# Optimization experiments

Measured on AMD Instinct MI355X. Metric: run time of the kernel, lower is better.

The kernel has to match this reference:

```python
import jax, jax.numpy as jnp
import numpy as np

SIZES = [(64, 32), (32, 16), (16, 8), (8, 16), (16, 32)]
BZ, T, D = 2048, 512, 64


def setup_inputs() -> dict:
    key = jax.random.key(0)
    ks = jax.random.split(key, 32)
    inp = {
        "X": jax.random.normal(ks[0], (BZ, T, D), jnp.float32),
        "missing_mask": (jax.random.uniform(ks[1], (BZ, T, D)) < 0.8).astype(jnp.float32),
        "imputation_latent": jax.random.normal(ks[2], (BZ, T, D), jnp.float32),
    }
    for i, (din, dh) in enumerate(SIZES):
        s = 1.0 / np.sqrt(dh)  # PyTorch RNNCell init range
        k = 3 + 4 * i
        inp[f"wih{i}"] = jax.random.uniform(ks[k], (3 * dh, din), jnp.float32, -s, s)
        inp[f"whh{i}"] = jax.random.uniform(ks[k + 1], (3 * dh, dh), jnp.float32, -s, s)
        inp[f"bih{i}"] = jax.random.uniform(ks[k + 2], (3 * dh,), jnp.float32, -s, s)
        inp[f"bhh{i}"] = jax.random.uniform(ks[k + 3], (3 * dh,), jnp.float32, -s, s)
    so = 1.0 / np.sqrt(32)
    inp["out_w"] = jax.random.uniform(ks[23], (D, 32), jnp.float32, -so, so)
    inp["out_b"] = jax.random.uniform(ks[24], (D,), jnp.float32, -so, so)
    return inp


def _gru_cell(x, h, wih, whh, bih, bhh):
    # PyTorch nn.GRUCell gate order: r, z, n
    gi = x @ wih.T + bih
    gh = h @ whh.T + bhh
    ir, iz, inn = jnp.split(gi, 3, axis=-1)
    hr, hz, hn = jnp.split(gh, 3, axis=-1)
    r = jax.nn.sigmoid(ir + hr)
    z = jax.nn.sigmoid(iz + hz)
    n = jnp.tanh(inn + r * hn)
    return (1.0 - z) * n + z * h


def _forward(X, missing_mask, imputation_latent, params, out_w, out_b):
    imputed = X * missing_mask + imputation_latent * (1.0 - missing_mask)
    xs = jnp.swapaxes(imputed, 0, 1)  # [T, B, D]
    bz = X.shape[0]
    h0 = tuple(jnp.zeros((bz, dh), X.dtype) for _, dh in SIZES)

    def step(hs, x):
        new = []
        inp_x = x
        for i, (wih, whh, bih, bhh) in enumerate(params):
            h = _gru_cell(inp_x, hs[i], wih, whh, bih, bhh)
            new.append(h)
            inp_x = h  # layer i+1 consumes the freshly-updated hidden state
        return tuple(new), new[-1]

    _, hcol = jax.lax.scan(step, h0, xs)  # [T, B, 32]
    hcol = jnp.swapaxes(hcol, 0, 1)  # [B, T, 32]
    return hcol @ out_w.T + out_b


def reference(X, missing_mask, imputation_latent,
              wih0, whh0, bih0, bhh0, wih1, whh1, bih1, bhh1,
              wih2, whh2, bih2, bhh2, wih3, whh3, bih3, bhh3,
              wih4, whh4, bih4, bhh4, out_w, out_b):
    params = [(wih0, whh0, bih0, bhh0), (wih1, whh1, bih1, bhh1),
              (wih2, whh2, bih2, bhh2), (wih3, whh3, bih3, bhh3),
              (wih4, whh4, bih4, bhh4)]
    return _forward(X, missing_mask, imputation_latent, params, out_w, out_b)
```

## Files before the change

### kernel.cpp

```cpp
#include <hip/hip_runtime.h>

typedef short s16x8 __attribute__((ext_vector_type(8)));
typedef short s16x4 __attribute__((ext_vector_type(4)));
typedef float f32x4 __attribute__((ext_vector_type(4)));
typedef unsigned int u32;
typedef unsigned short u16;

#define NT 512
#define DD 64
#define BB 8
#define NTH 512

#define CHUNK 1024

#define P2STRIDE (5*CHUNK)
#define PH0 0
#define PH1 CHUNK
#define PH2 (2*CHUNK)
#define PH3 (3*CHUNK)
#define PH4 (4*CHUNK)
#define FRTOT2 (2*P2STRIDE)
#define NSTEP2 517

#define PSTRIDE (7*CHUNK)
#define XIN0 0
#define H0C (2*CHUNK)
#define H1C (3*CHUNK)
#define H2C (4*CHUNK)
#define H3C (5*CHUNK)
#define H4C (6*CHUNK)
#define FRTOT (2*PSTRIDE)
#define NSTEP_FB 517

#define MFMA16(A,B,C) __builtin_amdgcn_mfma_f32_16x16x32_bf16(A,B,C,0,0,0)

__device__ __forceinline__ float sigf(float x){ return 1.0f/(1.0f+__expf(-x)); }
__device__ __forceinline__ float tanhf2(float x){ return 2.0f/(1.0f+__expf(-2.0f*x)) - 1.0f; }

__device__ __forceinline__ u16 f2bf(float f) {
  u32 u = __builtin_bit_cast(u32, f);
  return (u16)((u + 0x7fffu + ((u >> 16) & 1u)) >> 16);
}
__device__ __forceinline__ float bf2f(u16 h) {
  u32 u = ((u32)h) << 16;
  return __builtin_bit_cast(float, u);
}

__device__ __forceinline__ void soft_barrier() {
  asm volatile("s_waitcnt lgkmcnt(0)" ::: "memory");
  __builtin_amdgcn_s_barrier();
  asm volatile("" ::: "memory");
}

__device__ __forceinline__ u32 cvtpk_bf16(float a, float b) {
  u32 r;
  asm("v_cvt_pk_bf16_f32 %0, %1, %2" : "=v"(r) : "v"(a), "v"(b));
  return r;
}

__device__ __forceinline__ void load_wfrag(const float* __restrict__ W, int row0, int nrow, int din,
                                           int kbase, int lane, s16x8& hi, s16x8& lo)
{
  const int m = lane & 15, kb = lane >> 4;
#pragma unroll
  for (int e = 0; e < 8; ++e) {
    int k = kbase + kb*8 + e;
    float v = (m < nrow && k < din) ? W[(size_t)(row0 + m)*din + k] : 0.0f;
    u16 h = f2bf(v);
    hi[e] = (short)h;
    lo[e] = (short)f2bf(v - bf2f(h));
  }
}

__device__ __forceinline__ void read_b(const u16* base, int lane, s16x8& hi, s16x8& lo)
{
  const int off = ((lane >> 4) << 8) + ((lane & 15) << 3);
  hi = *(const s16x8*)(base + off);
  lo = *(const s16x8*)(base + off + 128);
}

__device__ __forceinline__ void combine_write2(
    f32x4 aR, f32x4 aZ, f32x4 aNi, f32x4 aNh,
    float (&hprev)[4], u16* hdst_base, int jbase, int nrow, int lane)
{
  const int bb = lane & 15, q = lane >> 4;
  float hv[4];
#pragma unroll
  for (int i = 0; i < 4; ++i) {
    float rr = sigf(aR[i]);
    float zz = sigf(aZ[i]);
    float nn = tanhf2(aNi[i] + rr*aNh[i]);
    hv[i] = (1.0f - zz)*nn + zz*hprev[i];
    hprev[i] = hv[i];
  }
  if (bb < 8 && q*4 < nrow) {
    const int j = jbase + q*4;
    u16* dst = hdst_base + ((j >> 3) << 8) + bb*8 + (j & 7);
    u32 p01 = cvtpk_bf16(hv[0], hv[1]);
    u32 p23 = cvtpk_bf16(hv[2], hv[3]);
    float h0 = __builtin_bit_cast(float, p01 << 16);
    float h1 = __builtin_bit_cast(float, p01 & 0xffff0000u);
    float h2 = __builtin_bit_cast(float, p23 << 16);
    float h3 = __builtin_bit_cast(float, p23 & 0xffff0000u);
    u32 q01 = cvtpk_bf16(hv[0]-h0, hv[1]-h1);
    u32 q23 = cvtpk_bf16(hv[2]-h2, hv[3]-h3);
    uint2 hp_; hp_.x = p01; hp_.y = p23;
    uint2 lp_; lp_.x = q01; lp_.y = q23;
    *(uint2*)dst = hp_;
    *(uint2*)(dst + 128) = lp_;
  }
}

__device__ __forceinline__ void combine_write(
    f32x4 aR, f32x4 aZ, f32x4 aNi, f32x4 aNh,
    float (&hprev)[4], u16* hdst_base, int jbase, int nrow, int lane)
{
  const int bb = lane & 15, q = lane >> 4;
  float hv[4];
#pragma unroll
  for (int i = 0; i < 4; ++i) {
    float rr = sigf(aR[i]);
    float zz = sigf(aZ[i]);
    float nn = tanhf2(aNi[i] + rr*aNh[i]);
    hv[i] = (1.0f - zz)*nn + zz*hprev[i];
    hprev[i] = hv[i];
  }
  if (bb < 8 && q*4 < nrow) {
    const int j = jbase + q*4;
    const int kb = j >> 3, e = j & 7;
    s16x4 hh, ll;
#pragma unroll
    for (int i = 0; i < 4; ++i) {
      u16 h = f2bf(hv[i]);
      hh[i] = (short)h;
      ll[i] = (short)f2bf(hv[i] - bf2f(h));
    }
    u16* dst = hdst_base + kb*256 + bb*8 + e;
    *(s16x4*)dst = hh;
    *(s16x4*)(dst + 128) = ll;
  }
}

__global__ __launch_bounds__(256)
void gi0_gemm(const float* __restrict__ X, const float* __restrict__ M, const float* __restrict__ L,
              const float* __restrict__ wih0, const float* __restrict__ bih0,
              const float* __restrict__ bhh0,
              float* __restrict__ gi)
{
  __shared__ u32 xs[128*65];
  const int tid = threadIdx.x;
  const int wv = tid >> 6, lane = tid & 63;
  const int q = lane >> 4;
  const int b = blockIdx.x >> 2;
  const int t0 = (blockIdx.x & 3) * 128;
  const size_t base = ((size_t)b*NT + t0)*DD;

  for (int i = tid; i < 128*64; i += 256) {
    float x = X[base+i], m = M[base+i], l = L[base+i];
    float v = x*m + l*(1.0f - m);
    u16 h = f2bf(v);
    u16 lo2 = f2bf(v - bf2f(h));
    const int t = i >> 6, d = i & 63;
    xs[t*65 + d] = (u32)h | ((u32)lo2 << 16);
  }

  s16x8 Ah[6][2], Al[6][2];
  f32x4 cb[6];
#pragma unroll
  for (int tile = 0; tile < 6; ++tile) {
#pragma unroll
    for (int c = 0; c < 2; ++c)
      load_wfrag(wih0, tile*16, 16, 64, c*32, lane, Ah[tile][c], Al[tile][c]);
#pragma unroll
    for (int i = 0; i < 4; ++i) {
      int row = tile*16 + q*4 + i;
      float bv = bih0[row];
      if (tile < 4) bv += bhh0[row];
      cb[tile][i] = bv;
    }
  }
  __syncthreads();

#pragma unroll
  for (int g2 = 0; g2 < 2; ++g2) {
    const int tloc = g2*64 + wv*16 + (lane & 15);
    s16x8 Bh[2], Bl[2];
#pragma unroll
    for (int c = 0; c < 2; ++c) {
      const u32* p = &xs[tloc*65 + c*32 + q*8];
#pragma unroll
      for (int e = 0; e < 8; ++e) {
        u32 v = p[e];
        Bh[c][e] = (short)(v & 0xffffu);
        Bl[c][e] = (short)(v >> 16);
      }
    }
    float* gp = gi + ((size_t)b*NT + t0 + tloc)*96 + q*4;
#pragma unroll
    for (int tile = 0; tile < 6; ++tile) {
      f32x4 acc = cb[tile];
#pragma unroll
      for (int c = 0; c < 2; ++c) {
        acc = MFMA16(Ah[tile][c], Bh[c], acc);
        acc = MFMA16(Ah[tile][c], Bl[c], acc);
        acc = MFMA16(Al[tile][c], Bh[c], acc);
      }
      *(f32x4*)(gp + tile*16) = acc;
    }
  }
}

__device__ __forceinline__ void wave_l0(
    const float* __restrict__ Whh, const float* __restrict__ bhh,
    const float* __restrict__ gi, int jbase,
    u16* FRu, int b0, int lane)
{
  s16x8 Ahh[3], Ahl[3];
#pragma unroll
  for (int g = 0; g < 3; ++g)
    load_wfrag(Whh, g*32 + jbase, 16, 32, 0, lane, Ahh[g], Ahl[g]);
  const int q = lane >> 4;
  f32x4 cNh;
#pragma unroll
  for (int i = 0; i < 4; ++i) cNh[i] = bhh[64 + jbase + q*4 + i];
  float hprev[4] = {0.f,0.f,0.f,0.f};

  const float* gp = gi + (size_t)(b0 + (lane & 7)) * ((size_t)NT*96) + jbase + q*4;
  f32x4 gR0, gZ0, gN0, gR1, gZ1, gN1;
  gR0 = *(const f32x4*)(gp); gZ0 = *(const f32x4*)(gp+32); gN0 = *(const f32x4*)(gp+64); gp += 96;
  gR1 = *(const f32x4*)(gp); gZ1 = *(const f32x4*)(gp+32); gN1 = *(const f32x4*)(gp+64); gp += 96;

  for (int s = 0; s < NSTEP2; ++s) {
    const int par = s & 1, rp = par ^ 1;
    f32x4 gR2 = {}, gZ2 = {}, gN2 = {};
    if (s + 2 < NT) {
      gR2 = *(const f32x4*)(gp); gZ2 = *(const f32x4*)(gp+32); gN2 = *(const f32x4*)(gp+64); gp += 96;
    }
    if (s < NT) {
      f32x4 aR = gR0, aZ = gZ0, aNi = gN0, aNh = cNh;
      s16x8 bh_, bl_;
      read_b(FRu + rp*P2STRIDE + PH0, lane, bh_, bl_);
      aR  = MFMA16(Ahh[0], bh_, aR);  aR  = MFMA16(Ahh[0], bl_, aR);  aR  = MFMA16(Ahl[0], bh_, aR);
      aZ  = MFMA16(Ahh[1], bh_, aZ);  aZ  = MFMA16(Ahh[1], bl_, aZ);  aZ  = MFMA16(Ahl[1], bh_, aZ);
      aNh = MFMA16(Ahh[2], bh_, aNh); aNh = MFMA16(Ahh[2], bl_, aNh); aNh = MFMA16(Ahl[2], bh_, aNh);
      combine_write2(aR, aZ, aNi, aNh, hprev, FRu + par*P2STRIDE + PH0, jbase, 16, lane);
    }
    gR0 = gR1; gZ0 = gZ1; gN0 = gN1;
    gR1 = gR2; gZ1 = gZ2; gN1 = gN2;
    soft_barrier();
  }
}

template<int DIN, int DH>
__device__ __forceinline__ void wave_mid(
    const float* __restrict__ Wih, const float* __restrict__ Whh,
    const float* __restrict__ bih, const float* __restrict__ bhh,
    int jbase, int xc, int hc, int s0, int s1,
    u16* FRu, int b0, int lane)
{
  const int nrow = (DH - jbase) < 16 ? (DH - jbase) : 16;
  s16x8 Axh[3], Axl[3], Ahh[3], Ahl[3];
#pragma unroll
  for (int g = 0; g < 3; ++g) {
    load_wfrag(Wih, g*DH + jbase, nrow, DIN, 0, lane, Axh[g], Axl[g]);
    load_wfrag(Whh, g*DH + jbase, nrow, DH, 0, lane, Ahh[g], Ahl[g]);
  }
  const int q = lane >> 4;
  f32x4 cR, cZ, cNi, cNh;
#pragma unroll
  for (int i = 0; i < 4; ++i) {
    int lr = q*4 + i;
    int j = jbase + lr;
    bool jr = lr < nrow;
    cR[i]  = jr ? bih[j] + bhh[j] : 0.f;
    cZ[i]  = jr ? bih[DH+j] + bhh[DH+j] : 0.f;
    cNi[i] = jr ? bih[2*DH+j] : 0.f;
    cNh[i] = jr ? bhh[2*DH+j] : 0.f;
  }
  float hprev[4] = {0.f,0.f,0.f,0.f};

  for (int s = 0; s < NSTEP2; ++s) {
    const int par = s & 1, rp = par ^ 1;
    if (s >= s0 && s <= s1) {
      f32x4 aR = cR, aZ = cZ, aNi = cNi, aNh = cNh;
      s16x8 bh_, bl_;
      read_b(FRu + rp*P2STRIDE + xc, lane, bh_, bl_);
      aR  = MFMA16(Axh[0], bh_, aR);  aR  = MFMA16(Axh[0], bl_, aR);  aR  = MFMA16(Axl[0], bh_, aR);
      aZ  = MFMA16(Axh[1], bh_, aZ);  aZ  = MFMA16(Axh[1], bl_, aZ);  aZ  = MFMA16(Axl[1], bh_, aZ);
      aNi = MFMA16(Axh[2], bh_, aNi); aNi = MFMA16(Axh[2], bl_, aNi); aNi = MFMA16(Axl[2], bh_, aNi);
      read_b(FRu + rp*P2STRIDE + hc, lane, bh_, bl_);
      aR  = MFMA16(Ahh[0], bh_, aR);  aR  = MFMA16(Ahh[0], bl_, aR);  aR  = MFMA16(Ahl[0], bh_, aR);
      aZ  = MFMA16(Ahh[1], bh_, aZ);  aZ  = MFMA16(Ahh[1], bl_, aZ);  aZ  = MFMA16(Ahl[1], bh_, aZ);
      aNh = MFMA16(Ahh[2], bh_, aNh); aNh = MFMA16(Ahh[2], bl_, aNh); aNh = MFMA16(Ahl[2], bh_, aNh);
      combine_write2(aR, aZ, aNi, aNh, hprev, FRu + par*P2STRIDE + hc, jbase, nrow, lane);
    }
    soft_barrier();
  }
}

__device__ __forceinline__ void wave_out2(
    const float* __restrict__ OW, const float* __restrict__ OBb,
    u16* FRu, float* __restrict__ out, int b0, int lane)
{
  s16x8 Oh[4], Ol[4];
  f32x4 cO[4];
  const int q = lane >> 4, bb = lane & 15;
#pragma unroll
  for (int t4 = 0; t4 < 4; ++t4) {
    load_wfrag(OW, t4*16, 16, 32, 0, lane, Oh[t4], Ol[t4]);
#pragma unroll
    for (int i = 0; i < 4; ++i) cO[t4][i] = OBb[t4*16 + q*4 + i];
  }
  float* op = out + ((size_t)(b0 + (bb & 7))*NT)*DD + q*4;

  for (int s = 0; s < NSTEP2; ++s) {
    const int rp = (s & 1) ^ 1;
    if (s >= 5) {
      s16x8 bh_, bl_;
      read_b(FRu + rp*P2STRIDE + PH4, lane, bh_, bl_);
#pragma unroll
      for (int t4 = 0; t4 < 4; ++t4) {
        f32x4 a_ = cO[t4];
        a_ = MFMA16(Oh[t4], bh_, a_); a_ = MFMA16(Oh[t4], bl_, a_); a_ = MFMA16(Ol[t4], bh_, a_);
        if (bb < 8) *(f32x4*)(op + t4*16) = a_;
      }
      op += DD;
    }
    soft_barrier();
  }
}

__global__ __launch_bounds__(NTH, 1)
void gru_rec(const float* __restrict__ gi,
             const float* __restrict__ whh0, const float* __restrict__ bhh0,
             const float* __restrict__ wih1, const float* __restrict__ whh1, const float* __restrict__ bih1, const float* __restrict__ bhh1,
             const float* __restrict__ wih2, const float* __restrict__ whh2, const float* __restrict__ bih2, const float* __restrict__ bhh2,
             const float* __restrict__ wih3, const float* __restrict__ whh3, const float* __restrict__ bih3, const float* __restrict__ bhh3,
             const float* __restrict__ wih4, const float* __restrict__ whh4, const float* __restrict__ bih4, const float* __restrict__ bhh4,
             const float* __restrict__ out_w, const float* __restrict__ out_b,
             float* __restrict__ out)
{
  __shared__ __align__(16) u16 FRu[FRTOT2];
  const int tid = threadIdx.x;
  const int w = tid >> 6, lane = tid & 63;
  const int b0 = blockIdx.x * BB;

  for (int i = tid; i < FRTOT2; i += NTH) FRu[i] = 0;
  __syncthreads();

  if (w == 0)
    wave_l0(whh0, bhh0, gi,  0, FRu, b0, lane);
  else if (w == 1)
    wave_l0(whh0, bhh0, gi, 16, FRu, b0, lane);
  else if (w == 2)
    wave_mid<32,16>(wih1,whh1,bih1,bhh1,  0, PH0, PH1, 1, 512, FRu, b0, lane);
  else if (w == 4)
    wave_mid<16, 8>(wih2,whh2,bih2,bhh2,  0, PH1, PH2, 2, 513, FRu, b0, lane);
  else if (w == 5)
    wave_mid< 8,16>(wih3,whh3,bih3,bhh3,  0, PH2, PH3, 3, 514, FRu, b0, lane);
  else if (w == 3)
    wave_mid<16,32>(wih4,whh4,bih4,bhh4,  0, PH3, PH4, 4, 515, FRu, b0, lane);
  else if (w == 6)
    wave_mid<16,32>(wih4,whh4,bih4,bhh4, 16, PH3, PH4, 4, 515, FRu, b0, lane);
  else
    wave_out2(out_w, out_b, FRu, out, b0, lane);
}

__device__ __forceinline__ void write_x(u16* FRu, int par, int w, int lane, float v)
{
  const int d = lane;
  const int chunk = d >> 5, kb = (d >> 3) & 3, e = d & 7;
  u16 h = f2bf(v);
  u16 l2 = f2bf(v - bf2f(h));
  u16* p = FRu + par*PSTRIDE + XIN0 + chunk*CHUNK + kb*256 + w*8 + e;
  p[0] = h; p[128] = l2;
}

template<int DIN, int DH, int NXC>
__device__ __forceinline__ void wave_gru_fb(
    const float* __restrict__ Wih, const float* __restrict__ Whh,
    const float* __restrict__ bih, const float* __restrict__ bhh,
    int jbase, int xc, int hc, int s0, int s1,
    u16* FRu, float* OST,
    const float* __restrict__ X, const float* __restrict__ Mm, const float* __restrict__ Ll,
    float* __restrict__ out, int b0, int w, int lane)
{
  const int nrow = (DH - jbase) < 16 ? (DH - jbase) : 16;
  s16x8 Axh[3][NXC], Axl[3][NXC], Ahh[3], Ahl[3];
#pragma unroll
  for (int g = 0; g < 3; ++g) {
#pragma unroll
    for (int c = 0; c < NXC; ++c)
      load_wfrag(Wih, g*DH + jbase, nrow, DIN, c*32, lane, Axh[g][c], Axl[g][c]);
    load_wfrag(Whh, g*DH + jbase, nrow, DH, 0, lane, Ahh[g], Ahl[g]);
  }
  f32x4 cR, cZ, cNi, cNh;
  {
    const int q = lane >> 4;
#pragma unroll
    for (int i = 0; i < 4; ++i) {
      int lr = q*4 + i;
      int j = jbase + lr;
      bool jr = lr < nrow;
      cR[i]  = jr ? bih[j] + bhh[j] : 0.f;
      cZ[i]  = jr ? bih[DH+j] + bhh[DH+j] : 0.f;
      cNi[i] = jr ? bih[2*DH+j] : 0.f;
      cNh[i] = jr ? bhh[2*DH+j] : 0.f;
    }
  }
  float hprev[4] = {0.f, 0.f, 0.f, 0.f};

  const size_t gbase = ((size_t)(b0 + w))*((size_t)NT*DD) + lane;
  float rx = X[gbase], rm = Mm[gbase], rl = Ll[gbase];
  write_x(FRu, 1, w, lane, rx*rm + rl*(1.0f - rm));
  rx = X[gbase + DD]; rm = Mm[gbase + DD]; rl = Ll[gbase + DD];
  __syncthreads();

  for (int s = 0; s < NSTEP_FB; ++s) {
    const int par = s & 1, rp = par ^ 1;
    float nx = 0.f, nm = 0.f, nl = 0.f;
    if (s <= 509) {
      size_t g = gbase + (size_t)(s+2)*DD;
      nx = X[g]; nm = Mm[g]; nl = Ll[g];
    }
    f32x4 aR = cR, aZ = cZ, aNi = cNi, aNh = cNh;
    const bool run = (s >= s0) && (s <= s1);
    if (run) {
      const u16* RB = FRu + rp*PSTRIDE;
      s16x8 bh_, bl_;
#pragma unroll
      for (int c = 0; c < NXC; ++c) {
        read_b(RB + xc + c*CHUNK, lane, bh_, bl_);
        aR  = MFMA16(Axh[0][c], bh_, aR);  aR  = MFMA16(Axh[0][c], bl_, aR);  aR  = MFMA16(Axl[0][c], bh_, aR);
        aZ  = MFMA16(Axh[1][c], bh_, aZ);  aZ  = MFMA16(Axh[1][c], bl_, aZ);  aZ  = MFMA16(Axl[1][c], bh_, aZ);
        aNi = MFMA16(Axh[2][c], bh_, aNi); aNi = MFMA16(Axh[2][c], bl_, aNi); aNi = MFMA16(Axl[2][c], bh_, aNi);
      }
      read_b(RB + hc, lane, bh_, bl_);
      aR  = MFMA16(Ahh[0], bh_, aR);  aR  = MFMA16(Ahh[0], bl_, aR);  aR  = MFMA16(Ahl[0], bh_, aR);
      aZ  = MFMA16(Ahh[1], bh_, aZ);  aZ  = MFMA16(Ahh[1], bl_, aZ);  aZ  = MFMA16(Ahl[1], bh_, aZ);
      aNh = MFMA16(Ahh[2], bh_, aNh); aNh = MFMA16(Ahh[2], bl_, aNh); aNh = MFMA16(Ahl[2], bh_, aNh);
    }
    __syncthreads();

    if (run)
      combine_write(aR, aZ, aNi, aNh, hprev, FRu + par*PSTRIDE + hc, jbase, nrow, lane);
    if (s >= 5)
      out[((size_t)(b0 + w)*NT + (s-5))*DD + lane] = OST[w*65 + lane];
    if (s <= 510) write_x(FRu, par, w, lane, rx*rm + rl*(1.0f - rm));
    rx = nx; rm = nm; rl = nl;
    __syncthreads();
  }
}

__device__ __forceinline__ void wave_out_fb(
    const float* __restrict__ OW, const float* __restrict__ OBb,
    u16* FRu, float* OST,
    const float* __restrict__ X, const float* __restrict__ Mm, const float* __restrict__ Ll,
    float* __restrict__ out, int b0, int w, int lane)
{
  s16x8 Oh[4], Ol[4];
  f32x4 cO[4];
#pragma unroll
  for (int t4 = 0; t4 < 4; ++t4) {
    load_wfrag(OW, t4*16, 16, 32, 0, lane, Oh[t4], Ol[t4]);
#pragma unroll
    for (int i = 0; i < 4; ++i) cO[t4][i] = OBb[t4*16 + (lane>>4)*4 + i];
  }
  const size_t gbase = ((size_t)(b0 + w))*((size_t)NT*DD) + lane;
  float rx = X[gbase], rm = Mm[gbase], rl = Ll[gbase];
  write_x(FRu, 1, w, lane, rx*rm + rl*(1.0f - rm));
  rx = X[gbase + DD]; rm = Mm[gbase + DD]; rl = Ll[gbase + DD];
  __syncthreads();

  for (int s = 0; s < NSTEP_FB; ++s) {
    const int par = s & 1, rp = par ^ 1;
    float nx = 0.f, nm = 0.f, nl = 0.f;
    if (s <= 509) { size_t g = gbase + (size_t)(s+2)*DD; nx = X[g]; nm = Mm[g]; nl = Ll[g]; }
    if (s >= 5) {
      s16x8 bh_, bl_;
      read_b(FRu + rp*PSTRIDE + H4C, lane, bh_, bl_);
      const int bb = lane & 15, q = lane >> 4;
#pragma unroll
      for (int t4 = 0; t4 < 4; ++t4) {
        f32x4 a_ = cO[t4];
        a_ = MFMA16(Oh[t4], bh_, a_); a_ = MFMA16(Oh[t4], bl_, a_); a_ = MFMA16(Ol[t4], bh_, a_);
        if (bb < 8) {
#pragma unroll
          for (int i = 0; i < 4; ++i) OST[bb*65 + t4*16 + q*4 + i] = a_[i];
        }
      }
    }
    __syncthreads();
    if (s >= 5)
      out[((size_t)(b0 + w)*NT + (s-5))*DD + lane] = OST[w*65 + lane];
    if (s <= 510) write_x(FRu, par, w, lane, rx*rm + rl*(1.0f - rm));
    rx = nx; rm = nm; rl = nl;
    __syncthreads();
  }
}

__global__ __launch_bounds__(NTH, 1)
void gru_mfma(const float* __restrict__ X, const float* __restrict__ M, const float* __restrict__ L,
              const float* __restrict__ wih0, const float* __restrict__ whh0, const float* __restrict__ bih0, const float* __restrict__ bhh0,
              const float* __restrict__ wih1, const float* __restrict__ whh1, const float* __restrict__ bih1, const float* __restrict__ bhh1,
              const float* __restrict__ wih2, const float* __restrict__ whh2, const float* __restrict__ bih2, const float* __restrict__ bhh2,
              const float* __restrict__ wih3, const float* __restrict__ whh3, const float* __restrict__ bih3, const float* __restrict__ bhh3,
              const float* __restrict__ wih4, const float* __restrict__ whh4, const float* __restrict__ bih4, const float* __restrict__ bhh4,
              const float* __restrict__ out_w, const float* __restrict__ out_b,
              float* __restrict__ out)
{
  __shared__ __align__(16) u16 FRu[FRTOT];
  __shared__ float OST[8*65];
  const int tid = threadIdx.x;
  const int w = tid >> 6, lane = tid & 63;
  const int b0 = blockIdx.x * BB;

  for (int i = tid; i < FRTOT; i += NTH) FRu[i] = 0;
  for (int i = tid; i < 8*65; i += NTH) OST[i] = 0.f;
  __syncthreads();

  if (w == 0)
    wave_gru_fb<64,32,2>(wih0,whh0,bih0,bhh0,  0, XIN0, H0C, 0, 511, FRu, OST, X,M,L, out, b0, w, lane);
  else if (w == 1)
    wave_gru_fb<64,32,2>(wih0,whh0,bih0,bhh0, 16, XIN0, H0C, 0, 511, FRu, OST, X,M,L, out, b0, w, lane);
  else if (w == 2)
    wave_gru_fb<32,16,1>(wih1,whh1,bih1,bhh1,  0, H0C,  H1C, 1, 512, FRu, OST, X,M,L, out, b0, w, lane);
  else if (w == 4)
    wave_gru_fb<16, 8,1>(wih2,whh2,bih2,bhh2,  0, H1C,  H2C, 2, 513, FRu, OST, X,M,L, out, b0, w, lane);
  else if (w == 5)
    wave_gru_fb< 8,16,1>(wih3,whh3,bih3,bhh3,  0, H2C,  H3C, 3, 514, FRu, OST, X,M,L, out, b0, w, lane);
  else if (w == 3)
    wave_gru_fb<16,32,1>(wih4,whh4,bih4,bhh4,  0, H3C,  H4C, 4, 515, FRu, OST, X,M,L, out, b0, w, lane);
  else if (w == 6)
    wave_gru_fb<16,32,1>(wih4,whh4,bih4,bhh4, 16, H3C,  H4C, 4, 515, FRu, OST, X,M,L, out, b0, w, lane);
  else
    wave_out_fb(out_w, out_b, FRu, OST, X,M,L, out, b0, w, lane);
}

extern "C" void kernel_launch(void* const* d_in, const int* in_sizes, int n_in,
                              void* d_out, int out_size, void* d_ws, size_t ws_size,
                              hipStream_t stream)
{
  const float* X  = (const float*)d_in[0];
  const float* M  = (const float*)d_in[1];
  const float* L  = (const float*)d_in[2];
  const float* wp[20];
  for (int i = 0; i < 20; ++i) wp[i] = (const float*)d_in[3 + i];
  const float* ow = (const float*)d_in[23];
  const float* ob = (const float*)d_in[24];
  float* out = (float*)d_out;

  const size_t gi_bytes = (size_t)2048 * NT * 96 * sizeof(float);
  if (ws_size >= gi_bytes) {
    float* gi = (float*)d_ws;
    gi0_gemm<<<dim3(2048*4), dim3(256), 0, stream>>>(X, M, L, wp[0], wp[2], wp[3], gi);
    gru_rec<<<dim3(2048 / BB), dim3(NTH), 0, stream>>>(
        gi, wp[1], wp[3],
        wp[4], wp[5], wp[6], wp[7],
        wp[8], wp[9], wp[10], wp[11],
        wp[12], wp[13], wp[14], wp[15],
        wp[16], wp[17], wp[18], wp[19],
        ow, ob, out);
  } else {
    gru_mfma<<<dim3(2048 / BB), dim3(NTH), 0, stream>>>(
        X, M, L,
        wp[0], wp[1], wp[2], wp[3],
        wp[4], wp[5], wp[6], wp[7],
        wp[8], wp[9], wp[10], wp[11],
        wp[12], wp[13], wp[14], wp[15],
        wp[16], wp[17], wp[18], wp[19],
        ow, ob, out);
  }
}
```

Baseline: 840.1 us.

## Split recurrence into 4-batch, 4-wave blocks with lane-swizzled gate combine

Each recurrent block now handles 4 batch rows with 4 waves instead of 8 rows with 8 waves, launching 512 blocks with two blocks per CU. Each wave now runs several layer tiles: layer 0 as two tiles, layers 1+2, layers 3 plus half of layer 4, and the other half of layer 4 plus the output projection. The combine step uses ds_swizzle so the upper half of the lanes processes accumulator rows 2-3, which avoids idle lanes when only 4 batch columns are live. The aim is to double the number of blocks and give more CUs work, at the cost of more serial MFMA work per wave on each timestep.

Result: slower. 1.016 ms (+21.0%).

```diff
diff --git a/kernel.cpp b/kernel.cpp
--- a/kernel.cpp
+++ b/kernel.cpp
@@ -8,7 +8,6 @@
 
 #define NT 512
 #define DD 64
-#define BB 8
 #define NTH 512
 
 #define CHUNK 1024
@@ -58,6 +57,11 @@
   return r;
 }
 
+__device__ __forceinline__ float swzf(float v) {
+  return __builtin_bit_cast(float,
+      __builtin_amdgcn_ds_swizzle(__builtin_bit_cast(int, v), 0x201F));
+}
+
 __device__ __forceinline__ void load_wfrag(const float* __restrict__ W, int row0, int nrow, int din,
                                            int kbase, int lane, s16x8& hi, s16x8& lo)
 {
@@ -79,66 +83,92 @@
   lo = *(const s16x8*)(base + off + 128);
 }
 
-__device__ __forceinline__ void combine_write2(
+template<bool NI_OWN>
+__device__ __forceinline__ void combine_split(
     f32x4 aR, f32x4 aZ, f32x4 aNi, f32x4 aNh,
-    float (&hprev)[4], u16* hdst_base, int jbase, int nrow, int lane)
+    float (&hp)[2], u16* dstC, int jt16, int nrow, int lane)
 {
   const int bb = lane & 15, q = lane >> 4;
-  float hv[4];
+  const bool hihalf = (bb & 8) != 0;
+  float sR2 = swzf(aR[2]), sR3 = swzf(aR[3]);
+  float sZ2 = swzf(aZ[2]), sZ3 = swzf(aZ[3]);
+  float sH2 = swzf(aNh[2]), sH3 = swzf(aNh[3]);
+  float r0 = hihalf ? sR2 : aR[0],  r1 = hihalf ? sR3 : aR[1];
+  float z0 = hihalf ? sZ2 : aZ[0],  z1 = hihalf ? sZ3 : aZ[1];
+  float nh0 = hihalf ? sH2 : aNh[0], nh1 = hihalf ? sH3 : aNh[1];
+  float ni0, ni1;
+  if (NI_OWN) {
+    ni0 = hihalf ? aNi[2] : aNi[0];
+    ni1 = hihalf ? aNi[3] : aNi[1];
+  } else {
+    float sN2 = swzf(aNi[2]), sN3 = swzf(aNi[3]);
+    ni0 = hihalf ? sN2 : aNi[0];
+    ni1 = hihalf ? sN3 : aNi[1];
+  }
+  float rr0 = sigf(r0), rr1 = sigf(r1);
+  float zz0 = sigf(z0), zz1 = sigf(z1);
+  float n0 = tanhf2(ni0 + rr0*nh0), n1 = tanhf2(ni1 + rr1*nh1);
+  float h0 = (1.0f - zz0)*n0 + zz0*hp[0];
+  float h1 = (1.0f - zz1)*n1 + zz1*hp[1];
+  hp[0] = h0; hp[1] = h1;
+  const int jj = q*4 + (hihalf ? 2 : 0);
+  if ((bb & 7) < 4 && jj < nrow) {
+    const int j = jt16 + jj;
+    u32 ph = cvtpk_bf16(h0, h1);
+    float f0 = h0 - __builtin_bit_cast(float, ph << 16);
+    float f1 = h1 - __builtin_bit_cast(float, ph & 0xffff0000u);
+    u32 pl = cvtpk_bf16(f0, f1);
+    u16* dst = dstC + ((j >> 3) << 8) + ((bb & 3) << 3) + (j & 7);
+    *(u32*)dst = ph;
+    *(u32*)(dst + 128) = pl;
+  }
+}
+
+struct WTile {
+  s16x8 Axh[3], Axl[3], Ahh[3], Ahl[3];
+  f32x4 cR, cZ, cNi, cNh;
+};
+
+__device__ __forceinline__ void load_tile(WTile& w,
+    const float* __restrict__ Wih, const float* __restrict__ Whh,
+    const float* __restrict__ bih, const float* __restrict__ bhh,
+    int jbase, int DH, int DIN, int nrow, int lane)
+{
+#pragma unroll
+  for (int g = 0; g < 3; ++g) {
+    load_wfrag(Wih, g*DH + jbase, nrow, DIN, 0, lane, w.Axh[g], w.Axl[g]);
+    load_wfrag(Whh, g*DH + jbase, nrow, DH, 0, lane, w.Ahh[g], w.Ahl[g]);
+  }
+  const int q = lane >> 4;
 #pragma unroll
   for (int i = 0; i < 4; ++i) {
-    float rr = sigf(aR[i]);
-    float zz = sigf(aZ[i]);
-    float nn = tanhf2(aNi[i] + rr*aNh[i]);
-    hv[i] = (1.0f - zz)*nn + zz*hprev[i];
-    hprev[i] = hv[i];
-  }
-  if (bb < 8 && q*4 < nrow) {
-    const int j = jbase + q*4;
-    u16* dst = hdst_base + ((j >> 3) << 8) + bb*8 + (j & 7);
-    u32 p01 = cvtpk_bf16(hv[0], hv[1]);
-    u32 p23 = cvtpk_bf16(hv[2], hv[3]);
-    float h0 = __builtin_bit_cast(float, p01 << 16);
-    float h1 = __builtin_bit_cast(float, p01 & 0xffff0000u);
-    float h2 = __builtin_bit_cast(float, p23 << 16);
-    float h3 = __builtin_bit_cast(float, p23 & 0xffff0000u);
-    u32 q01 = cvtpk_bf16(hv[0]-h0, hv[1]-h1);
-    u32 q23 = cvtpk_bf16(hv[2]-h2, hv[3]-h3);
-    uint2 hp_; hp_.x = p01; hp_.y = p23;
-    uint2 lp_; lp_.x = q01; lp_.y = q23;
-    *(uint2*)dst = hp_;
-    *(uint2*)(dst + 128) = lp_;
-  }
-}
-
-__device__ __forceinline__ void combine_write(
-    f32x4 aR, f32x4 aZ, f32x4 aNi, f32x4 aNh,
-    float (&hprev)[4], u16* hdst_base, int jbase, int nrow, int lane)
-{
-  const int bb = lane & 15, q = lane >> 4;
-  float hv[4];
-#pragma unroll
-  for (int i = 0; i < 4; ++i) {
-    float rr = sigf(aR[i]);
-    float zz = sigf(aZ[i]);
-    float nn = tanhf2(aNi[i] + rr*aNh[i]);
-    hv[i] = (1.0f - zz)*nn + zz*hprev[i];
-    hprev[i] = hv[i];
-  }
-  if (bb < 8 && q*4 < nrow) {
-    const int j = jbase + q*4;
-    const int kb = j >> 3, e = j & 7;
-    s16x4 hh, ll;
-#pragma unroll
-    for (int i = 0; i < 4; ++i) {
-      u16 h = f2bf(hv[i]);
-      hh[i] = (short)h;
-      ll[i] = (short)f2bf(hv[i] - bf2f(h));
-    }
-    u16* dst = hdst_base + kb*256 + bb*8 + e;
-    *(s16x4*)dst = hh;
-    *(s16x4*)(dst + 128) = ll;
-  }
+    int lr = q*4 + i, j = jbase + lr;
+    bool jr = lr < nrow;
+    w.cR[i]  = jr ? bih[j] + bhh[j] : 0.f;
+    w.cZ[i]  = jr ? bih[DH+j] + bhh[DH+j] : 0.f;
+    w.cNi[i] = jr ? bih[2*DH+j] : 0.f;
+    w.cNh[i] = jr ? bhh[2*DH+j] : 0.f;
+  }
+}
+
+__device__ __forceinline__ void do_mid_tile(const WTile& w,
+    const u16* bx, const u16* bhc, u16* dstC,
+    float (&hp)[2], int jt16, int nrow, int lane)
+{
+  s16x8 bh_, bl_;
+  read_b(bx, lane, bh_, bl_);
+  f32x4 aR  = MFMA16(w.Axh[0], bh_, w.cR);
+  aR  = MFMA16(w.Axh[0], bl_, aR);  aR  = MFMA16(w.Axl[0], bh_, aR);
+  f32x4 aZ  = MFMA16(w.Axh[1], bh_, w.cZ);
+  aZ  = MFMA16(w.Axh[1], bl_, aZ);  aZ  = MFMA16(w.Axl[1], bh_, aZ);
+  f32x4 aNi = MFMA16(w.Axh[2], bh_, w.cNi);
+  aNi = MFMA16(w.Axh[2], bl_, aNi); aNi = MFMA16(w.Axl[2], bh_, aNi);
+  read_b(bhc, lane, bh_, bl_);
+  aR  = MFMA16(w.Ahh[0], bh_, aR);  aR  = MFMA16(w.Ahh[0], bl_, aR);  aR  = MFMA16(w.Ahl[0], bh_, aR);
+  aZ  = MFMA16(w.Ahh[1], bh_, aZ);  aZ  = MFMA16(w.Ahh[1], bl_, aZ);  aZ  = MFMA16(w.Ahl[1], bh_, aZ);
+  f32x4 aNh = MFMA16(w.Ahh[2], bh_, w.cNh);
+  aNh = MFMA16(w.Ahh[2], bl_, aNh); aNh = MFMA16(w.Ahl[2], bh_, aNh);
+  combine_split<false>(aR, aZ, aNi, aNh, hp, dstC, jt16, nrow, lane);
 }
 
 __global__ __launch_bounds__(256)
@@ -210,98 +240,130 @@
   }
 }
 
-__device__ __forceinline__ void wave_l0(
-    const float* __restrict__ Whh, const float* __restrict__ bhh,
-    const float* __restrict__ gi, int jbase,
-    u16* FRu, int b0, int lane)
-{
-  s16x8 Ahh[3], Ahl[3];
-#pragma unroll
-  for (int g = 0; g < 3; ++g)
-    load_wfrag(Whh, g*32 + jbase, 16, 32, 0, lane, Ahh[g], Ahl[g]);
+__device__ void wv_l0(const float* __restrict__ whh0, const float* __restrict__ bhh0,
+                      const float* __restrict__ gi, u16* FR, int b0, int lane)
+{
+  s16x8 Ahh[2][3], Ahl[2][3];
+#pragma unroll
+  for (int jt = 0; jt < 2; ++jt)
+#pragma unroll
+    for (int g = 0; g < 3; ++g)
+      load_wfrag(whh0, g*32 + jt*16, 16, 32, 0, lane, Ahh[jt][g], Ahl[jt][g]);
   const int q = lane >> 4;
-  f32x4 cNh;
-#pragma unroll
-  for (int i = 0; i < 4; ++i) cNh[i] = bhh[64 + jbase + q*4 + i];
-  float hprev[4] = {0.f,0.f,0.f,0.f};
-
-  const float* gp = gi + (size_t)(b0 + (lane & 7)) * ((size_t)NT*96) + jbase + q*4;
-  f32x4 gR0, gZ0, gN0, gR1, gZ1, gN1;
-  gR0 = *(const f32x4*)(gp); gZ0 = *(const f32x4*)(gp+32); gN0 = *(const f32x4*)(gp+64); gp += 96;
-  gR1 = *(const f32x4*)(gp); gZ1 = *(const f32x4*)(gp+32); gN1 = *(const f32x4*)(gp+64); gp += 96;
+  f32x4 cNh[2];
+#pragma unroll
+  for (int jt = 0; jt < 2; ++jt)
+#pragma unroll
+    for (int i = 0; i < 4; ++i) cNh[jt][i] = bhh0[64 + jt*16 + q*4 + i];
+  float hp[2][2] = {{0.f,0.f},{0.f,0.f}};
+
+  const float* gp = gi + (size_t)(b0 + (lane & 3)) * ((size_t)NT*96) + q*4;
+  f32x4 g0[2][3], g1[2][3];
+#pragma unroll
+  for (int jt = 0; jt < 2; ++jt) {
+    g0[jt][0] = *(const f32x4*)(gp + jt*16);
+    g0[jt][1] = *(const f32x4*)(gp + 32 + jt*16);
+    g0[jt][2] = *(const f32x4*)(gp + 64 + jt*16);
+  }
+  gp += 96;
+#pragma unroll
+  for (int jt = 0; jt < 2; ++jt) {
+    g1[jt][0] = *(const f32x4*)(gp + jt*16);
+    g1[jt][1] = *(const f32x4*)(gp + 32 + jt*16);
+    g1[jt][2] = *(const f32x4*)(gp + 64 + jt*16);
+  }
+  gp += 96;
 
   for (int s = 0; s < NSTEP2; ++s) {
     const int par = s & 1, rp = par ^ 1;
-    f32x4 gR2 = {}, gZ2 = {}, gN2 = {};
+    f32x4 g2[2][3];
+#pragma unroll
+    for (int jt = 0; jt < 2; ++jt)
+#pragma unroll
+      for (int g = 0; g < 3; ++g) g2[jt][g] = f32x4{0.f,0.f,0.f,0.f};
     if (s + 2 < NT) {
-      gR2 = *(const f32x4*)(gp); gZ2 = *(const f32x4*)(gp+32); gN2 = *(const f32x4*)(gp+64); gp += 96;
+#pragma unroll
+      for (int jt = 0; jt < 2; ++jt) {
+        g2[jt][0] = *(const f32x4*)(gp + jt*16);
+        g2[jt][1] = *(const f32x4*)(gp + 32 + jt*16);
+        g2[jt][2] = *(const f32x4*)(gp + 64 + jt*16);
+      }
+      gp += 96;
     }
     if (s < NT) {
-      f32x4 aR = gR0, aZ = gZ0, aNi = gN0, aNh = cNh;
       s16x8 bh_, bl_;
-      read_b(FRu + rp*P2STRIDE + PH0, lane, bh_, bl_);
-      aR  = MFMA16(Ahh[0], bh_, aR);  aR  = MFMA16(Ahh[0], bl_, aR);  aR  = MFMA16(Ahl[0], bh_, aR);
-      aZ  = MFMA16(Ahh[1], bh_, aZ);  aZ  = MFMA16(Ahh[1], bl_, aZ);  aZ  = MFMA16(Ahl[1], bh_, aZ);
-      aNh = MFMA16(Ahh[2], bh_, aNh); aNh = MFMA16(Ahh[2], bl_, aNh); aNh = MFMA16(Ahl[2], bh_, aNh);
-      combine_write2(aR, aZ, aNi, aNh, hprev, FRu + par*P2STRIDE + PH0, jbase, 16, lane);
-    }
-    gR0 = gR1; gZ0 = gZ1; gN0 = gN1;
-    gR1 = gR2; gZ1 = gZ2; gN1 = gN2;
+      read_b(FR + rp*P2STRIDE + PH0, lane, bh_, bl_);
+#pragma unroll
+      for (int jt = 0; jt < 2; ++jt) {
+        f32x4 aR  = MFMA16(Ahh[jt][0], bh_, g0[jt][0]);
+        aR  = MFMA16(Ahh[jt][0], bl_, aR);  aR  = MFMA16(Ahl[jt][0], bh_, aR);
+        f32x4 aZ  = MFMA16(Ahh[jt][1], bh_, g0[jt][1]);
+        aZ  = MFMA16(Ahh[jt][1], bl_, aZ);  aZ  = MFMA16(Ahl[jt][1], bh_, aZ);
+        f32x4 aNh = MFMA16(Ahh[jt][2], bh_, cNh[jt]);
+        aNh = MFMA16(Ahh[jt][2], bl_, aNh); aNh = MFMA16(Ahl[jt][2], bh_, aNh);
+        combine_split<true>(aR, aZ, g0[jt][2], aNh, hp[jt],
+                            FR + par*P2STRIDE + PH0, jt*16, 16, lane);
+      }
+    }
+#pragma unroll
+    for (int jt = 0; jt < 2; ++jt)
+#pragma unroll
+      for (int g = 0; g < 3; ++g) { g0[jt][g] = g1[jt][g]; g1[jt][g] = g2[jt][g]; }
     soft_barrier();
   }
 }
 
-template<int DIN, int DH>
-__device__ __forceinline__ void wave_mid(
-    const float* __restrict__ Wih, const float* __restrict__ Whh,
-    const float* __restrict__ bih, const float* __restrict__ bhh,
-    int jbase, int xc, int hc, int s0, int s1,
-    u16* FRu, int b0, int lane)
-{
-  const int nrow = (DH - jbase) < 16 ? (DH - jbase) : 16;
-  s16x8 Axh[3], Axl[3], Ahh[3], Ahl[3];
-#pragma unroll
-  for (int g = 0; g < 3; ++g) {
-    load_wfrag(Wih, g*DH + jbase, nrow, DIN, 0, lane, Axh[g], Axl[g]);
-    load_wfrag(Whh, g*DH + jbase, nrow, DH, 0, lane, Ahh[g], Ahl[g]);
-  }
-  const int q = lane >> 4;
-  f32x4 cR, cZ, cNi, cNh;
-#pragma unroll
-  for (int i = 0; i < 4; ++i) {
-    int lr = q*4 + i;
-    int j = jbase + lr;
-    bool jr = lr < nrow;
-    cR[i]  = jr ? bih[j] + bhh[j] : 0.f;
-    cZ[i]  = jr ? bih[DH+j] + bhh[DH+j] : 0.f;
-    cNi[i] = jr ? bih[2*DH+j] : 0.f;
-    cNh[i] = jr ? bhh[2*DH+j] : 0.f;
-  }
-  float hprev[4] = {0.f,0.f,0.f,0.f};
-
+__device__ void wv_l1_l2(
+    const float* __restrict__ wih1, const float* __restrict__ whh1,
+    const float* __restrict__ bih1, const float* __restrict__ bhh1,
+    const float* __restrict__ wih2, const float* __restrict__ whh2,
+    const float* __restrict__ bih2, const float* __restrict__ bhh2,
+    u16* FR, int lane)
+{
+  WTile t1, t2;
+  load_tile(t1, wih1, whh1, bih1, bhh1, 0, 16, 32, 16, lane);
+  load_tile(t2, wih2, whh2, bih2, bhh2, 0,  8, 16,  8, lane);
+  float hp1[2] = {0.f,0.f}, hp2[2] = {0.f,0.f};
   for (int s = 0; s < NSTEP2; ++s) {
     const int par = s & 1, rp = par ^ 1;
-    if (s >= s0 && s <= s1) {
-      f32x4 aR = cR, aZ = cZ, aNi = cNi, aNh = cNh;
-      s16x8 bh_, bl_;
-      read_b(FRu + rp*P2STRIDE + xc, lane, bh_, bl_);
-      aR  = MFMA16(Axh[0], bh_, aR);  aR  = MFMA16(Axh[0], bl_, aR);  aR  = MFMA16(Axl[0], bh_, aR);
-      aZ  = MFMA16(Axh[1], bh_, aZ);  aZ  = MFMA16(Axh[1], bl_, aZ);  aZ  = MFMA16(Axl[1], bh_, aZ);
-      aNi = MFMA16(Axh[2], bh_, aNi); aNi = MFMA16(Axh[2], bl_, aNi); aNi = MFMA16(Axl[2], bh_, aNi);
-      read_b(FRu + rp*P2STRIDE + hc, lane, bh_, bl_);
-      aR  = MFMA16(Ahh[0], bh_, aR);  aR  = MFMA16(Ahh[0], bl_, aR);  aR  = MFMA16(Ahl[0], bh_, aR);
-      aZ  = MFMA16(Ahh[1], bh_, aZ);  aZ  = MFMA16(Ahh[1], bl_, aZ);  aZ  = MFMA16(Ahl[1], bh_, aZ);
-      aNh = MFMA16(Ahh[2], bh_, aNh); aNh = MFMA16(Ahh[2], bl_, aNh); aNh = MFMA16(Ahl[2], bh_, aNh);
-      combine_write2(aR, aZ, aNi, aNh, hprev, FRu + par*P2STRIDE + hc, jbase, nrow, lane);
-    }
+    const u16* R = FR + rp*P2STRIDE;
+    u16* W = FR + par*P2STRIDE;
+    if (s >= 1 && s <= 512) do_mid_tile(t1, R+PH0, R+PH1, W+PH1, hp1, 0, 16, lane);
+    if (s >= 2 && s <= 513) do_mid_tile(t2, R+PH1, R+PH2, W+PH2, hp2, 0,  8, lane);
     soft_barrier();
   }
 }
 
-__device__ __forceinline__ void wave_out2(
+__device__ void wv_l3_l4b(
+    const float* __restrict__ wih3, const float* __restrict__ whh3,
+    const float* __restrict__ bih3, const float* __restrict__ bhh3,
+    const float* __restrict__ wih4, const float* __restrict__ whh4,
+    const float* __restrict__ bih4, const float* __restrict__ bhh4,
+    u16* FR, int lane)
+{
+  WTile t3, t4b;
+  load_tile(t3,  wih3, whh3, bih3, bhh3,  0, 16,  8, 16, lane);
+  load_tile(t4b, wih4, whh4, bih4, bhh4, 16, 32, 16, 16, lane);
+  float hp3[2] = {0.f,0.f}, hp4[2] = {0.f,0.f};
+  for (int s = 0; s < NSTEP2; ++s) {
+    const int par = s & 1, rp = par ^ 1;
+    const u16* R = FR + rp*P2STRIDE;
+    u16* W = FR + par*P2STRIDE;
+    if (s >= 3 && s <= 514) do_mid_tile(t3,  R+PH2, R+PH3, W+PH3, hp3,  0, 16, lane);
+    if (s >= 4 && s <= 515) do_mid_tile(t4b, R+PH3, R+PH4, W+PH4, hp4, 16, 16, lane);
+    soft_barrier();
+  }
+}
+
+__device__ void wv_l4a_out(
+    const float* __restrict__ wih4, const float* __restrict__ whh4,
+    const float* __restrict__ bih4, const float* __restrict__ bhh4,
     const float* __restrict__ OW, const float* __restrict__ OBb,
-    u16* FRu, float* __restrict__ out, int b0, int lane)
-{
+    u16* FR, float* __restrict__ out, int b0, int lane)
+{
+  WTile t4a;
+  load_tile(t4a, wih4, whh4, bih4, bhh4, 0, 32, 16, 16, lane);
+  float hp4[2] = {0.f,0.f};
   s16x8 Oh[4], Ol[4];
   f32x4 cO[4];
   const int q = lane >> 4, bb = lane & 15;
@@ -311,59 +373,84 @@
 #pragma unroll
     for (int i = 0; i < 4; ++i) cO[t4][i] = OBb[t4*16 + q*4 + i];
   }
-  float* op = out + ((size_t)(b0 + (bb & 7))*NT)*DD + q*4;
+  float* ob = out + ((size_t)(b0 + (bb & 3))*NT)*DD + q*4;
 
   for (int s = 0; s < NSTEP2; ++s) {
-    const int rp = (s & 1) ^ 1;
+    const int par = s & 1, rp = par ^ 1;
+    const u16* R = FR + rp*P2STRIDE;
+    u16* W = FR + par*P2STRIDE;
+    if (s >= 4 && s <= 515) do_mid_tile(t4a, R+PH3, R+PH4, W+PH4, hp4, 0, 16, lane);
     if (s >= 5) {
       s16x8 bh_, bl_;
-      read_b(FRu + rp*P2STRIDE + PH4, lane, bh_, bl_);
+      read_b(R + PH4, lane, bh_, bl_);
+      float* op = ob + (size_t)(s-5)*DD;
 #pragma unroll
       for (int t4 = 0; t4 < 4; ++t4) {
         f32x4 a_ = cO[t4];
         a_ = MFMA16(Oh[t4], bh_, a_); a_ = MFMA16(Oh[t4], bl_, a_); a_ = MFMA16(Ol[t4], bh_, a_);
-        if (bb < 8) *(f32x4*)(op + t4*16) = a_;
+        if (bb < 4) *(f32x4*)(op + t4*16) = a_;
       }
-      op += DD;
     }
     soft_barrier();
   }
 }
 
-__global__ __launch_bounds__(NTH, 1)
-void gru_rec(const float* __restrict__ gi,
-             const float* __restrict__ whh0, const float* __restrict__ bhh0,
-             const float* __restrict__ wih1, const float* __restrict__ whh1, const float* __restrict__ bih1, const float* __restrict__ bhh1,
-             const float* __restrict__ wih2, const float* __restrict__ whh2, const float* __restrict__ bih2, const float* __restrict__ bhh2,
-             const float* __restrict__ wih3, const float* __restrict__ whh3, const float* __restrict__ bih3, const float* __restrict__ bhh3,
-             const float* __restrict__ wih4, const float* __restrict__ whh4, const float* __restrict__ bih4, const float* __restrict__ bhh4,
-             const float* __restrict__ out_w, const float* __restrict__ out_b,
-             float* __restrict__ out)
+__global__ __launch_bounds__(256, 2)
+void gru_rec4(const float* __restrict__ gi,
+              const float* __restrict__ whh0, const float* __restrict__ bhh0,
+              const float* __restrict__ wih1, const float* __restrict__ whh1, const float* __restrict__ bih1, const float* __restrict__ bhh1,
+              const float* __restrict__ wih2, const float* __restrict__ whh2, const float* __restrict__ bih2, const float* __restrict__ bhh2,
+              const float* __restrict__ wih3, const float* __restrict__ whh3, const float* __restrict__ bih3, const float* __restrict__ bhh3,
+              const float* __restrict__ wih4, const float* __restrict__ whh4, const float* __restrict__ bih4, const float* __restrict__ bhh4,
+              const float* __restrict__ out_w, const float* __restrict__ out_b,
+              float* __restrict__ out)
 {
   __shared__ __align__(16) u16 FRu[FRTOT2];
   const int tid = threadIdx.x;
   const int w = tid >> 6, lane = tid & 63;
-  const int b0 = blockIdx.x * BB;
-
-  for (int i = tid; i < FRTOT2; i += NTH) FRu[i] = 0;
+  const int b0 = blockIdx.x * 4;
+
+  for (int i = tid; i < FRTOT2; i += 256) FRu[i] = 0;
   __syncthreads();
 
   if (w == 0)
-    wave_l0(whh0, bhh0, gi,  0, FRu, b0, lane);
+    wv_l0(whh0, bhh0, gi, FRu, b0, lane);
   else if (w == 1)
-    wave_l0(whh0, bhh0, gi, 16, FRu, b0, lane);
+    wv_l1_l2(wih1,whh1,bih1,bhh1, wih2,whh2,bih2,bhh2, FRu, lane);
   else if (w == 2)
-    wave_mid<32,16>(wih1,whh1,bih1,bhh1,  0, PH0, PH1, 1, 512, FRu, b0, lane);
-  else if (w == 4)
-    wave_mid<16, 8>(wih2,whh2,bih2,bhh2,  0, PH1, PH2, 2, 513, FRu, b0, lane);
-  else if (w == 5)
-    wave_mid< 8,16>(wih3,whh3,bih3,bhh3,  0, PH2, PH3, 3, 514, FRu, b0, lane);
-  else if (w == 3)
-    wave_mid<16,32>(wih4,whh4,bih4,bhh4,  0, PH3, PH4, 4, 515, FRu, b0, lane);
-  else if (w == 6)
-    wave_mid<16,32>(wih4,whh4,bih4,bhh4, 16, PH3, PH4, 4, 515, FRu, b0, lane);
+    wv_l4a_out(wih4,whh4,bih4,bhh4, out_w, out_b, FRu, out, b0, lane);
   else
-    wave_out2(out_w, out_b, FRu, out, b0, lane);
+    wv_l3_l4b(wih3,whh3,bih3,bhh3, wih4,whh4,bih4,bhh4, FRu, lane);
+}
+
+__device__ __forceinline__ void combine_write(
+    f32x4 aR, f32x4 aZ, f32x4 aNi, f32x4 aNh,
+    float (&hprev)[4], u16* hdst_base, int jbase, int nrow, int lane)
+{
+  const int bb = lane & 15, q = lane >> 4;
+  float hv[4];
+#pragma unroll
+  for (int i = 0; i < 4; ++i) {
+    float rr = sigf(aR[i]);
+    float zz = sigf(aZ[i]);
+    float nn = tanhf2(aNi[i] + rr*aNh[i]);
+    hv[i] = (1.0f - zz)*nn + zz*hprev[i];
+    hprev[i] = hv[i];
+  }
+  if (bb < 8 && q*4 < nrow) {
+    const int j = jbase + q*4;
+    const int kb = j >> 3, e = j & 7;
+    s16x4 hh, ll;
+#pragma unroll
+    for (int i = 0; i < 4; ++i) {
+      u16 h = f2bf(hv[i]);
+      hh[i] = (short)h;
+      ll[i] = (short)f2bf(hv[i] - bf2f(h));
+    }
+    u16* dst = hdst_base + kb*256 + bb*8 + e;
+    *(s16x4*)dst = hh;
+    *(s16x4*)(dst + 128) = ll;
+  }
 }
 
 __device__ __forceinline__ void write_x(u16* FRu, int par, int w, int lane, float v)
@@ -513,7 +600,7 @@
   __shared__ float OST[8*65];
   const int tid = threadIdx.x;
   const int w = tid >> 6, lane = tid & 63;
-  const int b0 = blockIdx.x * BB;
+  const int b0 = blockIdx.x * 8;
 
   for (int i = tid; i < FRTOT; i += NTH) FRu[i] = 0;
   for (int i = tid; i < 8*65; i += NTH) OST[i] = 0.f;
@@ -554,7 +641,7 @@
   if (ws_size >= gi_bytes) {
     float* gi = (float*)d_ws;
     gi0_gemm<<<dim3(2048*4), dim3(256), 0, stream>>>(X, M, L, wp[0], wp[2], wp[3], gi);
-    gru_rec<<<dim3(2048 / BB), dim3(NTH), 0, stream>>>(
+    gru_rec4<<<dim3(512), dim3(256), 0, stream>>>(
         gi, wp[1], wp[3],
         wp[4], wp[5], wp[6], wp[7],
         wp[8], wp[9], wp[10], wp[11],
@@ -562,7 +649,7 @@
         wp[16], wp[17], wp[18], wp[19],
         ow, ob, out);
   } else {
-    gru_mfma<<<dim3(2048 / BB), dim3(NTH), 0, stream>>>(
+    gru_mfma<<<dim3(256), dim3(NTH), 0, stream>>>(
         X, M, L,
         wp[0], wp[1], wp[2], wp[3],
         wp[4], wp[5], wp[6], wp[7],
```
